# Kernel tuning notes

Measured on AMD Instinct MI355X. Metric: run time of the kernel, lower is better.

The kernel has to match this reference:

```python
import jax, jax.numpy as jnp
import numpy as np

B, S, D_IN, D_QK, D_V = 4, 4096, 1024, 64, 64

def setup_inputs() -> dict:
    key = jax.random.key(0)
    ks = jax.random.split(key, 8)
    sd = 1.0 / np.sqrt(D_IN)
    return {
        "X": jax.random.normal(ks[0], (B, S, D_IN), dtype=jnp.float32),
        "mask": jnp.ones((B, S, 1), dtype=jnp.float32),
        "Wq": jax.random.uniform(ks[1], (D_IN, D_QK), jnp.float32, -sd, sd),
        "bq": jax.random.uniform(ks[2], (D_QK,), jnp.float32, -sd, sd),
        "Wk": jax.random.uniform(ks[3], (D_IN, D_QK), jnp.float32, -sd, sd),
        "bk": jax.random.uniform(ks[4], (D_QK,), jnp.float32, -sd, sd),
        "Wv": jax.random.uniform(ks[5], (D_IN, D_V), jnp.float32, -sd, sd),
        "bv": jax.random.uniform(ks[6], (D_V,), jnp.float32, -sd, sd),
    }

def reference(X, mask, Wq, bq, Wk, bk, Wv, bv):
    # ReLU-activated projections (no head split, no 1/sqrt(d) scaling)
    q = jax.nn.relu(jnp.einsum('bsd,df->bsf', X, Wq) + bq)   # [B,S,D_QK]
    k = jax.nn.relu(jnp.einsum('bsd,df->bsf', X, Wk) + bk)   # [B,S,D_QK]
    v = jax.nn.relu(jnp.einsum('bsd,df->bsf', X, Wv) + bv)   # [B,S,D_V]
    scores = jax.nn.softmax(jnp.einsum('bqf,bkf->bqk', q, k), axis=-1)  # [B,S,S]
    return jnp.einsum('bqk,bkf->bqf', scores, v) * mask       # mask applied AFTER AV
```

## Files before the change

kernel.cpp:

```cpp
#include <hip/hip_runtime.h>


typedef short s16x8 __attribute__((ext_vector_type(8)));
typedef float fx4   __attribute__((ext_vector_type(4)));
typedef unsigned short u16x4 __attribute__((ext_vector_type(4)));

#define LOG2E 1.4426950408889634f

__device__ __forceinline__ unsigned short f2bf(float x) {
    unsigned int u = __float_as_uint(x);
    u += 0x7FFFu + ((u >> 16) & 1u);
    return (unsigned short)(u >> 16);
}
__device__ __forceinline__ float bf2f(unsigned short b) {
    return __uint_as_float(((unsigned int)b) << 16);
}

__global__ __launch_bounds__(256) void prep_w_kernel(
    const float* __restrict__ Wq, const float* __restrict__ Wk, const float* __restrict__ Wv,
    unsigned short* __restrict__ wt_hi, unsigned short* __restrict__ wt_lo)
{
    int idx = blockIdx.x * 256 + threadIdx.x;
    int y = idx >> 16;
    int r = idx & 65535;
    int k = r >> 6;
    int c = r & 63;
    const float* W = (y == 0) ? Wq : (y == 1) ? Wk : Wv;
    float x = W[r];
    unsigned short h = f2bf(x);
    unsigned short l = f2bf(x - bf2f(h));
    int o = (y * 64 + c) * 1024 + k;
    wt_hi[o] = h; wt_lo[o] = l;
}

__global__ __launch_bounds__(256, 4) void proj_kernel(
    const float* __restrict__ X,
    const unsigned short* __restrict__ wt_hi, const unsigned short* __restrict__ wt_lo,
    const float* __restrict__ bq, const float* __restrict__ bk, const float* __restrict__ bv,
    unsigned short* __restrict__ q_hi, unsigned short* __restrict__ q_lo,
    unsigned short* __restrict__ k_bf, unsigned short* __restrict__ vt_g)
{
    __shared__ __align__(16) unsigned short a_hi[64][72];
    __shared__ __align__(16) unsigned short a_lo[64][72];
    __shared__ __align__(16) unsigned short b_hi[64][72];
    __shared__ __align__(16) unsigned short b_lo[64][72];

    const int tid  = threadIdx.x;
    const int lane = tid & 63;
    const int w    = tid >> 6;
    const int quad = lane >> 4;
    const int l15  = lane & 15;
    const int y    = blockIdx.x;
    const int m0   = blockIdx.y * 64;

    fx4 acc[4];
    #pragma unroll
    for (int nt = 0; nt < 4; nt++)
        acc[nt] = (fx4){0.f, 0.f, 0.f, 0.f};

    for (int kc = 0; kc < 16; kc++) {
        #pragma unroll
        for (int i = 0; i < 4; i++) {
            int c = tid + i * 256;
            int row = c >> 4;
            int off = (c & 15) * 4;
            const float* src = X + (size_t)(m0 + row) * 1024 + kc * 64 + off;
            fx4 xv = *(const fx4*)src;
            unsigned short h0 = f2bf(xv.x), h1 = f2bf(xv.y), h2 = f2bf(xv.z), h3 = f2bf(xv.w);
            unsigned short l0 = f2bf(xv.x - bf2f(h0)), l1 = f2bf(xv.y - bf2f(h1));
            unsigned short l2 = f2bf(xv.z - bf2f(h2)), l3 = f2bf(xv.w - bf2f(h3));
            *(u16x4*)&a_hi[row][off] = (u16x4){h0, h1, h2, h3};
            *(u16x4*)&a_lo[row][off] = (u16x4){l0, l1, l2, l3};
        }
        #pragma unroll
        for (int i = 0; i < 2; i++) {
            int c = tid + i * 256;
            int row = c >> 3;
            int off = (c & 7) * 8;
            size_t g = (size_t)(y * 64 + row) * 1024 + kc * 64 + off;
            *(s16x8*)&b_hi[row][off] = *(const s16x8*)(wt_hi + g);
            *(s16x8*)&b_lo[row][off] = *(const s16x8*)(wt_lo + g);
        }
        __syncthreads();

        s16x8 ah[2], al[2];
        #pragma unroll
        for (int ks = 0; ks < 2; ks++) {
            int r = w * 16 + l15;
            ah[ks] = *(const s16x8*)&a_hi[r][ks * 32 + quad * 8];
            al[ks] = *(const s16x8*)&a_lo[r][ks * 32 + quad * 8];
        }
        #pragma unroll
        for (int nt = 0; nt < 4; nt++) {
            #pragma unroll
            for (int ks = 0; ks < 2; ks++) {
                s16x8 bh = *(const s16x8*)&b_hi[nt * 16 + l15][ks * 32 + quad * 8];
                s16x8 bl = *(const s16x8*)&b_lo[nt * 16 + l15][ks * 32 + quad * 8];
                acc[nt] = __builtin_amdgcn_mfma_f32_16x16x32_bf16(ah[ks], bh, acc[nt], 0, 0, 0);
                acc[nt] = __builtin_amdgcn_mfma_f32_16x16x32_bf16(ah[ks], bl, acc[nt], 0, 0, 0);
                acc[nt] = __builtin_amdgcn_mfma_f32_16x16x32_bf16(al[ks], bh, acc[nt], 0, 0, 0);
            }
        }
        __syncthreads();
    }

    const float* bias = (y == 0) ? bq : (y == 1) ? bk : bv;
    const int b   = m0 >> 12;
    const int s0b = m0 & 4095;
    unsigned short* vtr = (unsigned short*)&a_hi[0][0];

    #pragma unroll
    for (int nt = 0; nt < 4; nt++) {
        int col = nt * 16 + l15;
        float bb = bias[col];
        int rloc = w * 16 + quad * 4;
        #pragma unroll
        for (int r = 0; r < 4; r++) {
            float v = acc[nt][r] + bb;
            v = fmaxf(v, 0.f);
            size_t grow = (size_t)(m0 + rloc + r);
            if (y == 0) {
                unsigned short h = f2bf(v);
                unsigned short l = f2bf(v - bf2f(h));
                q_hi[grow * 64 + col] = h;
                q_lo[grow * 64 + col] = l;
            } else if (y == 1) {
                k_bf[grow * 64 + col] = f2bf(v);
            } else {
                vtr[col * 72 + rloc + r] = f2bf(v);
            }
        }
    }
    if (y == 2) {
        __syncthreads();
        #pragma unroll
        for (int i = 0; i < 2; i++) {
            int c = tid + i * 256;
            int row = c >> 3;
            int off = (c & 7) * 8;
            s16x8 vv = *(const s16x8*)&vtr[row * 72 + off];
            *(s16x8*)(vt_g + (size_t)(b * 64 + row) * 4096 + s0b + off) = vv;
        }
    }
}

__global__ __launch_bounds__(256) void attn_kernel(
    const unsigned short* __restrict__ q_hi, const unsigned short* __restrict__ q_lo,
    const unsigned short* __restrict__ k_bf, const unsigned short* __restrict__ vt_g,
    float* __restrict__ pO, float* __restrict__ pL)
{
    __shared__ __align__(16) unsigned short kt[64][72];
    __shared__ __align__(16) unsigned short vt[64][72];
    __shared__ __align__(16) unsigned short pt[4][16][72];

    const int tid  = threadIdx.x;
    const int lane = tid & 63;
    const int w    = tid >> 6;
    const int quad = lane >> 4;
    const int l15  = lane & 15;
    const int idx  = blockIdx.x;
    const int qt   = idx & 63;
    const int ck   = (idx >> 6) & 3;
    const int b    = idx >> 8;
    const int q0   = qt * 64;

    const size_t qoff = ((size_t)b * 4096 + q0 + w * 16 + l15) * 64 + quad * 8;
    s16x8 qh0 = *(const s16x8*)(q_hi + qoff);
    s16x8 qh1 = *(const s16x8*)(q_hi + qoff + 32);
    s16x8 ql0 = *(const s16x8*)(q_lo + qoff);
    s16x8 ql1 = *(const s16x8*)(q_lo + qoff + 32);

    fx4 accO[4];
    #pragma unroll
    for (int nt = 0; nt < 4; nt++) accO[nt] = (fx4){0.f, 0.f, 0.f, 0.f};
    float lpart[4] = {0.f, 0.f, 0.f, 0.f};

    const unsigned short* kgb = k_bf + (size_t)b * 4096 * 64;
    const unsigned short* vgb = vt_g + (size_t)b * 64 * 4096;

    for (int it = ck * 16; it < ck * 16 + 16; it++) {
        const unsigned short* kg = kgb + (size_t)it * 4096;
        #pragma unroll
        for (int i = 0; i < 2; i++) {
            int c = tid + i * 256;
            int row = c >> 3;
            int off = (c & 7) * 8;
            *(s16x8*)&kt[row][off] = *(const s16x8*)(kg + c * 8);
            *(s16x8*)&vt[row][off] = *(const s16x8*)(vgb + (size_t)row * 4096 + it * 64 + off);
        }
        __syncthreads();

        fx4 sc[4];
        #pragma unroll
        for (int nt = 0; nt < 4; nt++) sc[nt] = (fx4){0.f, 0.f, 0.f, 0.f};
        #pragma unroll
        for (int nt = 0; nt < 4; nt++) {
            s16x8 k0 = *(const s16x8*)&kt[nt * 16 + l15][quad * 8];
            s16x8 k1 = *(const s16x8*)&kt[nt * 16 + l15][32 + quad * 8];
            sc[nt] = __builtin_amdgcn_mfma_f32_16x16x32_bf16(qh0, k0, sc[nt], 0, 0, 0);
            sc[nt] = __builtin_amdgcn_mfma_f32_16x16x32_bf16(ql0, k0, sc[nt], 0, 0, 0);
            sc[nt] = __builtin_amdgcn_mfma_f32_16x16x32_bf16(qh1, k1, sc[nt], 0, 0, 0);
            sc[nt] = __builtin_amdgcn_mfma_f32_16x16x32_bf16(ql1, k1, sc[nt], 0, 0, 0);
        }

        #pragma unroll
        for (int nt = 0; nt < 4; nt++) {
            #pragma unroll
            for (int r = 0; r < 4; r++) {
                float p = __builtin_amdgcn_exp2f(sc[nt][r] * LOG2E);
                unsigned short pb = f2bf(p);
                lpart[r] += bf2f(pb);
                pt[w][quad * 4 + r][nt * 16 + l15] = pb;
            }
        }

        s16x8 pa0 = *(const s16x8*)&pt[w][l15][quad * 8];
        s16x8 pa1 = *(const s16x8*)&pt[w][l15][32 + quad * 8];
        #pragma unroll
        for (int nt = 0; nt < 4; nt++) {
            s16x8 v0 = *(const s16x8*)&vt[nt * 16 + l15][quad * 8];
            s16x8 v1 = *(const s16x8*)&vt[nt * 16 + l15][32 + quad * 8];
            accO[nt] = __builtin_amdgcn_mfma_f32_16x16x32_bf16(pa0, v0, accO[nt], 0, 0, 0);
            accO[nt] = __builtin_amdgcn_mfma_f32_16x16x32_bf16(pa1, v1, accO[nt], 0, 0, 0);
        }
        __syncthreads();
    }

    #pragma unroll
    for (int r = 0; r < 4; r++) {
        float v = lpart[r];
        #pragma unroll
        for (int o = 1; o < 16; o <<= 1) v += __shfl_xor(v, o);
        lpart[r] = v;
    }
    #pragma unroll
    for (int r = 0; r < 4; r++) {
        int qrow = q0 + w * 16 + quad * 4 + r;
        size_t grow = (size_t)b * 4096 + qrow;
        #pragma unroll
        for (int nt = 0; nt < 4; nt++)
            pO[((size_t)ck * 16384 + grow) * 64 + nt * 16 + l15] = accO[nt][r];
        if (l15 == 0)
            pL[(size_t)ck * 16384 + grow] = lpart[r];
    }
}

__global__ __launch_bounds__(256) void combine_kernel(
    const float* __restrict__ pO, const float* __restrict__ pL,
    const float* __restrict__ mask, float* __restrict__ out)
{
    int idx = blockIdx.x * 256 + threadIdx.x;
    int q  = idx >> 4;
    int dg = idx & 15;
    fx4 s = (fx4){0.f, 0.f, 0.f, 0.f};
    float l = 0.f;
    #pragma unroll
    for (int c = 0; c < 4; c++) {
        s += *(const fx4*)(pO + ((size_t)c * 16384 + q) * 64 + dg * 4);
        l += pL[(size_t)c * 16384 + q];
    }
    float scale = mask[q] / l;
    *(fx4*)(out + (size_t)q * 64 + dg * 4) = s * scale;
}

extern "C" void kernel_launch(void* const* d_in, const int* in_sizes, int n_in,
                              void* d_out, int out_size, void* d_ws, size_t ws_size,
                              hipStream_t stream)
{
    const float* X    = (const float*)d_in[0];
    const float* mask = (const float*)d_in[1];
    const float* Wq   = (const float*)d_in[2];
    const float* bq   = (const float*)d_in[3];
    const float* Wk   = (const float*)d_in[4];
    const float* bk   = (const float*)d_in[5];
    const float* Wv   = (const float*)d_in[6];
    const float* bv   = (const float*)d_in[7];
    float* out = (float*)d_out;

    char* ws = (char*)d_ws;
    unsigned short* q_hi  = (unsigned short*)(ws);
    unsigned short* q_lo  = (unsigned short*)(ws + (size_t)(2u << 20));
    unsigned short* k_bf  = (unsigned short*)(ws + (size_t)(4u << 20));
    unsigned short* vt_g  = (unsigned short*)(ws + (size_t)(6u << 20));
    unsigned short* wt_hi = (unsigned short*)(ws + (size_t)(8u << 20));
    unsigned short* wt_lo = (unsigned short*)(ws + (size_t)(8u << 20) + 393216);
    float*          pO    = (float*)(ws + (size_t)(9u << 20));
    float*          pL    = (float*)(ws + (size_t)(25u << 20));

    hipLaunchKernelGGL(prep_w_kernel, dim3(768), dim3(256), 0, stream,
                       Wq, Wk, Wv, wt_hi, wt_lo);
    hipLaunchKernelGGL(proj_kernel, dim3(3, 256), dim3(256), 0, stream,
                       X, wt_hi, wt_lo, bq, bk, bv, q_hi, q_lo, k_bf, vt_g);
    hipLaunchKernelGGL(attn_kernel, dim3(1024), dim3(256), 0, stream,
                       q_hi, q_lo, k_bf, vt_g, pO, pL);
    hipLaunchKernelGGL(combine_kernel, dim3(1024), dim3(256), 0, stream,
                       pO, pL, mask, out);
}
```

Measured before the change: 185.2 us.

## Prefetch projection tiles, widen proj blocks, split attention keys eightfold with bf16 partials

The projection kernel now runs 512 threads per block, with each wave computing half the output columns. It prefetches the next X and weight chunk into registers while computing the current one, which drops one barrier per iteration. The attention kernel splits keys into 8 chunks instead of 4, giving more blocks, and processes each 64-key tile in two 32-key halves to cut register and LDS use. Partial outputs are stored as bf16 to halve write and read traffic in the combine step, at some precision cost. Combine work grows to summing 8 partials per row.

```diff
diff --git a/kernel.cpp b/kernel.cpp
--- a/kernel.cpp
+++ b/kernel.cpp
@@ -33,15 +33,14 @@
     wt_hi[o] = h; wt_lo[o] = l;
 }
 
-__global__ __launch_bounds__(256, 4) void proj_kernel(
+__global__ __launch_bounds__(512, 6) void proj_kernel(
     const float* __restrict__ X,
     const unsigned short* __restrict__ wt_hi, const unsigned short* __restrict__ wt_lo,
     const float* __restrict__ bq, const float* __restrict__ bk, const float* __restrict__ bv,
     unsigned short* __restrict__ q_hi, unsigned short* __restrict__ q_lo,
     unsigned short* __restrict__ k_bf, unsigned short* __restrict__ vt_g)
 {
-    __shared__ __align__(16) unsigned short a_hi[64][72];
-    __shared__ __align__(16) unsigned short a_lo[64][72];
+    __shared__ __align__(16) unsigned short a_buf[2][64][72];
     __shared__ __align__(16) unsigned short b_hi[64][72];
     __shared__ __align__(16) unsigned short b_lo[64][72];
 
@@ -50,70 +49,86 @@
     const int w    = tid >> 6;
     const int quad = lane >> 4;
     const int l15  = lane & 15;
+    const int rs   = w & 3;
+    const int ch   = w >> 2;
     const int y    = blockIdx.x;
     const int m0   = blockIdx.y * 64;
 
-    fx4 acc[4];
-    #pragma unroll
-    for (int nt = 0; nt < 4; nt++)
-        acc[nt] = (fx4){0.f, 0.f, 0.f, 0.f};
+    fx4 acc[2];
+    acc[0] = (fx4){0.f, 0.f, 0.f, 0.f};
+    acc[1] = (fx4){0.f, 0.f, 0.f, 0.f};
+
+    const int xrow = tid >> 4;
+    const int xoff = (tid & 15) * 4;
+    const int wrow = tid >> 3;
+    const int woff = (tid & 7) * 8;
+
+    fx4   xr[2];
+    s16x8 wrh, wrl;
+    #pragma unroll
+    for (int i = 0; i < 2; i++)
+        xr[i] = *(const fx4*)(X + (size_t)(m0 + xrow + i * 32) * 1024 + xoff);
+    {
+        size_t g = (size_t)(y * 64 + wrow) * 1024 + woff;
+        wrh = *(const s16x8*)(wt_hi + g);
+        wrl = *(const s16x8*)(wt_lo + g);
+    }
 
     for (int kc = 0; kc < 16; kc++) {
-        #pragma unroll
-        for (int i = 0; i < 4; i++) {
-            int c = tid + i * 256;
-            int row = c >> 4;
-            int off = (c & 15) * 4;
-            const float* src = X + (size_t)(m0 + row) * 1024 + kc * 64 + off;
-            fx4 xv = *(const fx4*)src;
+        if (kc) __syncthreads();
+        #pragma unroll
+        for (int i = 0; i < 2; i++) {
+            fx4 xv = xr[i];
             unsigned short h0 = f2bf(xv.x), h1 = f2bf(xv.y), h2 = f2bf(xv.z), h3 = f2bf(xv.w);
             unsigned short l0 = f2bf(xv.x - bf2f(h0)), l1 = f2bf(xv.y - bf2f(h1));
             unsigned short l2 = f2bf(xv.z - bf2f(h2)), l3 = f2bf(xv.w - bf2f(h3));
-            *(u16x4*)&a_hi[row][off] = (u16x4){h0, h1, h2, h3};
-            *(u16x4*)&a_lo[row][off] = (u16x4){l0, l1, l2, l3};
-        }
-        #pragma unroll
-        for (int i = 0; i < 2; i++) {
-            int c = tid + i * 256;
-            int row = c >> 3;
-            int off = (c & 7) * 8;
-            size_t g = (size_t)(y * 64 + row) * 1024 + kc * 64 + off;
-            *(s16x8*)&b_hi[row][off] = *(const s16x8*)(wt_hi + g);
-            *(s16x8*)&b_lo[row][off] = *(const s16x8*)(wt_lo + g);
-        }
+            *(u16x4*)&a_buf[0][xrow + i * 32][xoff] = (u16x4){h0, h1, h2, h3};
+            *(u16x4*)&a_buf[1][xrow + i * 32][xoff] = (u16x4){l0, l1, l2, l3};
+        }
+        *(s16x8*)&b_hi[wrow][woff] = wrh;
+        *(s16x8*)&b_lo[wrow][woff] = wrl;
         __syncthreads();
 
+        if (kc < 15) {
+            #pragma unroll
+            for (int i = 0; i < 2; i++)
+                xr[i] = *(const fx4*)(X + (size_t)(m0 + xrow + i * 32) * 1024 + (kc + 1) * 64 + xoff);
+            size_t g = (size_t)(y * 64 + wrow) * 1024 + (kc + 1) * 64 + woff;
+            wrh = *(const s16x8*)(wt_hi + g);
+            wrl = *(const s16x8*)(wt_lo + g);
+        }
+
         s16x8 ah[2], al[2];
         #pragma unroll
         for (int ks = 0; ks < 2; ks++) {
-            int r = w * 16 + l15;
-            ah[ks] = *(const s16x8*)&a_hi[r][ks * 32 + quad * 8];
-            al[ks] = *(const s16x8*)&a_lo[r][ks * 32 + quad * 8];
-        }
-        #pragma unroll
-        for (int nt = 0; nt < 4; nt++) {
+            int r = rs * 16 + l15;
+            ah[ks] = *(const s16x8*)&a_buf[0][r][ks * 32 + quad * 8];
+            al[ks] = *(const s16x8*)&a_buf[1][r][ks * 32 + quad * 8];
+        }
+        #pragma unroll
+        for (int nt = 0; nt < 2; nt++) {
             #pragma unroll
             for (int ks = 0; ks < 2; ks++) {
-                s16x8 bh = *(const s16x8*)&b_hi[nt * 16 + l15][ks * 32 + quad * 8];
-                s16x8 bl = *(const s16x8*)&b_lo[nt * 16 + l15][ks * 32 + quad * 8];
+                s16x8 bh = *(const s16x8*)&b_hi[ch * 32 + nt * 16 + l15][ks * 32 + quad * 8];
+                s16x8 bl = *(const s16x8*)&b_lo[ch * 32 + nt * 16 + l15][ks * 32 + quad * 8];
                 acc[nt] = __builtin_amdgcn_mfma_f32_16x16x32_bf16(ah[ks], bh, acc[nt], 0, 0, 0);
                 acc[nt] = __builtin_amdgcn_mfma_f32_16x16x32_bf16(ah[ks], bl, acc[nt], 0, 0, 0);
                 acc[nt] = __builtin_amdgcn_mfma_f32_16x16x32_bf16(al[ks], bh, acc[nt], 0, 0, 0);
             }
         }
-        __syncthreads();
-    }
+    }
+    __syncthreads();
 
     const float* bias = (y == 0) ? bq : (y == 1) ? bk : bv;
     const int b   = m0 >> 12;
     const int s0b = m0 & 4095;
-    unsigned short* vtr = (unsigned short*)&a_hi[0][0];
-
-    #pragma unroll
-    for (int nt = 0; nt < 4; nt++) {
-        int col = nt * 16 + l15;
+    unsigned short* vtr = &a_buf[0][0][0];
+
+    #pragma unroll
+    for (int nt = 0; nt < 2; nt++) {
+        int col = ch * 32 + nt * 16 + l15;
         float bb = bias[col];
-        int rloc = w * 16 + quad * 4;
+        int rloc = rs * 16 + quad * 4;
         #pragma unroll
         for (int r = 0; r < 4; r++) {
             float v = acc[nt][r] + bb;
@@ -133,36 +148,30 @@
     }
     if (y == 2) {
         __syncthreads();
-        #pragma unroll
-        for (int i = 0; i < 2; i++) {
-            int c = tid + i * 256;
-            int row = c >> 3;
-            int off = (c & 7) * 8;
-            s16x8 vv = *(const s16x8*)&vtr[row * 72 + off];
-            *(s16x8*)(vt_g + (size_t)(b * 64 + row) * 4096 + s0b + off) = vv;
-        }
-    }
-}
-
-__global__ __launch_bounds__(256) void attn_kernel(
+        int row = tid >> 3;
+        int off = (tid & 7) * 8;
+        s16x8 vv = *(const s16x8*)&vtr[row * 72 + off];
+        *(s16x8*)(vt_g + (size_t)(b * 64 + row) * 4096 + s0b + off) = vv;
+    }
+}
+
+__global__ __launch_bounds__(256, 6) void attn_kernel(
     const unsigned short* __restrict__ q_hi, const unsigned short* __restrict__ q_lo,
     const unsigned short* __restrict__ k_bf, const unsigned short* __restrict__ vt_g,
-    float* __restrict__ pO, float* __restrict__ pL)
+    unsigned short* __restrict__ pOb, float* __restrict__ pL)
 {
     __shared__ __align__(16) unsigned short kt[64][72];
     __shared__ __align__(16) unsigned short vt[64][72];
-    __shared__ __align__(16) unsigned short pt[4][16][72];
+    __shared__ __align__(16) unsigned short pt[4][16][40];
 
     const int tid  = threadIdx.x;
     const int lane = tid & 63;
     const int w    = tid >> 6;
     const int quad = lane >> 4;
     const int l15  = lane & 15;
-    const int idx  = blockIdx.x;
-    const int qt   = idx & 63;
-    const int ck   = (idx >> 6) & 3;
-    const int b    = idx >> 8;
-    const int q0   = qt * 64;
+    const int ck   = blockIdx.y;
+    const int b    = blockIdx.z;
+    const int q0   = blockIdx.x * 64;
 
     const size_t qoff = ((size_t)b * 4096 + q0 + w * 16 + l15) * 64 + quad * 8;
     s16x8 qh0 = *(const s16x8*)(q_hi + qoff);
@@ -173,65 +182,60 @@
     fx4 accO[4];
     #pragma unroll
     for (int nt = 0; nt < 4; nt++) accO[nt] = (fx4){0.f, 0.f, 0.f, 0.f};
-    float lpart[4] = {0.f, 0.f, 0.f, 0.f};
+    float lsum[4] = {0.f, 0.f, 0.f, 0.f};
 
     const unsigned short* kgb = k_bf + (size_t)b * 4096 * 64;
     const unsigned short* vgb = vt_g + (size_t)b * 64 * 4096;
 
-    for (int it = ck * 16; it < ck * 16 + 16; it++) {
+    const int srow = tid >> 3;
+    const int soff = (tid & 7) * 8;
+
+    for (int it = ck * 8; it < ck * 8 + 8; it++) {
         const unsigned short* kg = kgb + (size_t)it * 4096;
         #pragma unroll
         for (int i = 0; i < 2; i++) {
-            int c = tid + i * 256;
-            int row = c >> 3;
-            int off = (c & 7) * 8;
-            *(s16x8*)&kt[row][off] = *(const s16x8*)(kg + c * 8);
-            *(s16x8*)&vt[row][off] = *(const s16x8*)(vgb + (size_t)row * 4096 + it * 64 + off);
+            int row = srow + i * 32;
+            *(s16x8*)&kt[row][soff] = *(const s16x8*)(kg + (size_t)row * 64 + soff);
+            *(s16x8*)&vt[row][soff] = *(const s16x8*)(vgb + (size_t)row * 4096 + it * 64 + soff);
         }
         __syncthreads();
 
-        fx4 sc[4];
-        #pragma unroll
-        for (int nt = 0; nt < 4; nt++) sc[nt] = (fx4){0.f, 0.f, 0.f, 0.f};
-        #pragma unroll
-        for (int nt = 0; nt < 4; nt++) {
-            s16x8 k0 = *(const s16x8*)&kt[nt * 16 + l15][quad * 8];
-            s16x8 k1 = *(const s16x8*)&kt[nt * 16 + l15][32 + quad * 8];
-            sc[nt] = __builtin_amdgcn_mfma_f32_16x16x32_bf16(qh0, k0, sc[nt], 0, 0, 0);
-            sc[nt] = __builtin_amdgcn_mfma_f32_16x16x32_bf16(ql0, k0, sc[nt], 0, 0, 0);
-            sc[nt] = __builtin_amdgcn_mfma_f32_16x16x32_bf16(qh1, k1, sc[nt], 0, 0, 0);
-            sc[nt] = __builtin_amdgcn_mfma_f32_16x16x32_bf16(ql1, k1, sc[nt], 0, 0, 0);
-        }
-
-        #pragma unroll
-        for (int nt = 0; nt < 4; nt++) {
+        #pragma unroll
+        for (int kh = 0; kh < 2; kh++) {
             #pragma unroll
-            for (int r = 0; r < 4; r++) {
-                float p = __builtin_amdgcn_exp2f(sc[nt][r] * LOG2E);
-                unsigned short pb = f2bf(p);
-                lpart[r] += bf2f(pb);
-                pt[w][quad * 4 + r][nt * 16 + l15] = pb;
+            for (int nt2 = 0; nt2 < 2; nt2++) {
+                int key = kh * 32 + nt2 * 16 + l15;
+                s16x8 k0 = *(const s16x8*)&kt[key][quad * 8];
+                s16x8 k1 = *(const s16x8*)&kt[key][32 + quad * 8];
+                fx4 sc = (fx4){0.f, 0.f, 0.f, 0.f};
+                sc = __builtin_amdgcn_mfma_f32_16x16x32_bf16(qh0, k0, sc, 0, 0, 0);
+                sc = __builtin_amdgcn_mfma_f32_16x16x32_bf16(ql0, k0, sc, 0, 0, 0);
+                sc = __builtin_amdgcn_mfma_f32_16x16x32_bf16(qh1, k1, sc, 0, 0, 0);
+                sc = __builtin_amdgcn_mfma_f32_16x16x32_bf16(ql1, k1, sc, 0, 0, 0);
+                #pragma unroll
+                for (int r = 0; r < 4; r++) {
+                    float p = __builtin_amdgcn_exp2f(sc[r] * LOG2E);
+                    unsigned short pb = f2bf(p);
+                    lsum[r] += bf2f(pb);
+                    pt[w][quad * 4 + r][nt2 * 16 + l15] = pb;
+                }
             }
-        }
-
-        s16x8 pa0 = *(const s16x8*)&pt[w][l15][quad * 8];
-        s16x8 pa1 = *(const s16x8*)&pt[w][l15][32 + quad * 8];
-        #pragma unroll
-        for (int nt = 0; nt < 4; nt++) {
-            s16x8 v0 = *(const s16x8*)&vt[nt * 16 + l15][quad * 8];
-            s16x8 v1 = *(const s16x8*)&vt[nt * 16 + l15][32 + quad * 8];
-            accO[nt] = __builtin_amdgcn_mfma_f32_16x16x32_bf16(pa0, v0, accO[nt], 0, 0, 0);
-            accO[nt] = __builtin_amdgcn_mfma_f32_16x16x32_bf16(pa1, v1, accO[nt], 0, 0, 0);
+            s16x8 pa = *(const s16x8*)&pt[w][l15][quad * 8];
+            #pragma unroll
+            for (int nt = 0; nt < 4; nt++) {
+                s16x8 vf = *(const s16x8*)&vt[nt * 16 + l15][kh * 32 + quad * 8];
+                accO[nt] = __builtin_amdgcn_mfma_f32_16x16x32_bf16(pa, vf, accO[nt], 0, 0, 0);
+            }
         }
         __syncthreads();
     }
 
     #pragma unroll
     for (int r = 0; r < 4; r++) {
-        float v = lpart[r];
+        float v = lsum[r];
         #pragma unroll
         for (int o = 1; o < 16; o <<= 1) v += __shfl_xor(v, o);
-        lpart[r] = v;
+        lsum[r] = v;
     }
     #pragma unroll
     for (int r = 0; r < 4; r++) {
@@ -239,14 +243,14 @@
         size_t grow = (size_t)b * 4096 + qrow;
         #pragma unroll
         for (int nt = 0; nt < 4; nt++)
-            pO[((size_t)ck * 16384 + grow) * 64 + nt * 16 + l15] = accO[nt][r];
+            pOb[((size_t)ck * 16384 + grow) * 64 + nt * 16 + l15] = f2bf(accO[nt][r]);
         if (l15 == 0)
-            pL[(size_t)ck * 16384 + grow] = lpart[r];
+            pL[(size_t)ck * 16384 + grow] = lsum[r];
     }
 }
 
 __global__ __launch_bounds__(256) void combine_kernel(
-    const float* __restrict__ pO, const float* __restrict__ pL,
+    const unsigned short* __restrict__ pOb, const float* __restrict__ pL,
     const float* __restrict__ mask, float* __restrict__ out)
 {
     int idx = blockIdx.x * 256 + threadIdx.x;
@@ -255,8 +259,12 @@
     fx4 s = (fx4){0.f, 0.f, 0.f, 0.f};
     float l = 0.f;
     #pragma unroll
-    for (int c = 0; c < 4; c++) {
-        s += *(const fx4*)(pO + ((size_t)c * 16384 + q) * 64 + dg * 4);
+    for (int c = 0; c < 8; c++) {
+        u16x4 h = *(const u16x4*)(pOb + ((size_t)c * 16384 + q) * 64 + dg * 4);
+        s.x += bf2f(h.x);
+        s.y += bf2f(h.y);
+        s.z += bf2f(h.z);
+        s.w += bf2f(h.w);
         l += pL[(size_t)c * 16384 + q];
     }
     float scale = mask[q] / l;
@@ -284,15 +292,15 @@
     unsigned short* vt_g  = (unsigned short*)(ws + (size_t)(6u << 20));
     unsigned short* wt_hi = (unsigned short*)(ws + (size_t)(8u << 20));
     unsigned short* wt_lo = (unsigned short*)(ws + (size_t)(8u << 20) + 393216);
-    float*          pO    = (float*)(ws + (size_t)(9u << 20));
+    unsigned short* pOb   = (unsigned short*)(ws + (size_t)(9u << 20));
     float*          pL    = (float*)(ws + (size_t)(25u << 20));
 
     hipLaunchKernelGGL(prep_w_kernel, dim3(768), dim3(256), 0, stream,
                        Wq, Wk, Wv, wt_hi, wt_lo);
-    hipLaunchKernelGGL(proj_kernel, dim3(3, 256), dim3(256), 0, stream,
+    hipLaunchKernelGGL(proj_kernel, dim3(3, 256), dim3(512), 0, stream,
                        X, wt_hi, wt_lo, bq, bk, bv, q_hi, q_lo, k_bf, vt_g);
-    hipLaunchKernelGGL(attn_kernel, dim3(1024), dim3(256), 0, stream,
-                       q_hi, q_lo, k_bf, vt_g, pO, pL);
+    hipLaunchKernelGGL(attn_kernel, dim3(64, 8, 4), dim3(256), 0, stream,
+                       q_hi, q_lo, k_bf, vt_g, pOb, pL);
     hipLaunchKernelGGL(combine_kernel, dim3(1024), dim3(256), 0, stream,
-                       pO, pL, mask, out);
-}
+                       pOb, pL, mask, out);
+}
```

Result: faster. 177.6 us (-4.1%).
